# Kernel tuning notes

Hardware: AMD Instinct MI355X
Metric: run time of the kernel (lower is better)

The kernel has to match this reference:

```python
import jax, jax.numpy as jnp
import numpy as np
import math

H = 512
NH = 8
HD = H // NH


def _lin_params(key, out_dim, in_dim):
    k1, k2 = jax.random.split(key)
    bound = 1.0 / math.sqrt(in_dim)
    w = jax.random.uniform(k1, (out_dim, in_dim), minval=-bound, maxval=bound, dtype=jnp.float32)
    b = jax.random.uniform(k2, (out_dim,), minval=-bound, maxval=bound, dtype=jnp.float32)
    return w, b


def setup_inputs() -> dict:
    key = jax.random.key(0)
    ks = jax.random.split(key, 16)
    B, L = 8, 1024
    inp = {
        'hidden_states': jax.random.normal(ks[0], (B, L, H), dtype=jnp.float32),
        'text': jax.random.normal(ks[1], (B, L, H), dtype=jnp.float32),
    }
    names = ['q_img', 'k_img', 'v_img', 'q_txt', 'k_txt', 'v_txt', 'out_img', 'out_txt']
    for i, n in enumerate(names):
        w, b = _lin_params(ks[2 + i], H, H)
        inp['w_' + n] = w
        inp['b_' + n] = b
    wcat, bcat = _lin_params(ks[10], H, 2 * H)
    inp['w_cat'] = wcat
    inp['b_cat'] = bcat
    # nn.MultiheadAttention params: in_proj [3H, H], out_proj [H, H]
    inp['in_proj_w'] = jax.random.normal(ks[11], (3 * H, H), dtype=jnp.float32) * (1.0 / math.sqrt(H))
    inp['in_proj_b'] = jnp.zeros((3 * H,), dtype=jnp.float32)
    pw, pb = _lin_params(ks[12], H, H)
    inp['out_proj_w'] = pw
    inp['out_proj_b'] = pb
    return inp


def _lin(x, w, b):
    return x @ w.T + b


def _heads(x):
    B, L, _ = x.shape
    return x.reshape(B, L, NH, HD).transpose(0, 2, 1, 3)  # [B, NH, L, HD]


def _attn(q, k, v):
    # q,k,v: [B, NH, L, HD]; dropout is identity in eval mode
    scores = jnp.einsum('bhqd,bhkd->bhqk', q, k) / math.sqrt(HD)
    probs = jax.nn.softmax(scores, axis=-1)
    ctx = jnp.einsum('bhqk,bhkd->bhqd', probs, v)
    B, _, L, _ = ctx.shape
    return ctx.transpose(0, 2, 1, 3).reshape(B, L, H)


def reference(hidden_states, text,
              w_q_img, b_q_img, w_k_img, b_k_img, w_v_img, b_v_img,
              w_q_txt, b_q_txt, w_k_txt, b_k_txt, w_v_txt, b_v_txt,
              w_out_img, b_out_img, w_out_txt, b_out_txt,
              w_cat, b_cat, in_proj_w, in_proj_b, out_proj_w, out_proj_b):
    q_img = _heads(_lin(hidden_states, w_q_img, b_q_img))
    k_img = _heads(_lin(hidden_states, w_k_img, b_k_img))
    v_img = _heads(_lin(hidden_states, w_v_img, b_v_img))
    q_txt = _heads(_lin(text, w_q_txt, b_q_txt))
    k_txt = _heads(_lin(text, w_k_txt, b_k_txt))
    v_txt = _heads(_lin(text, w_v_txt, b_v_txt))

    ctx_img = _attn(q_img, k_img, v_img)
    ctx_txt = _attn(q_txt, k_txt, v_txt)
    ctx_it = _attn(q_img, k_txt, v_txt)
    ctx_ti = _attn(q_txt, k_img, v_img)

    out_img = _lin((ctx_img + ctx_it) * 0.5, w_out_img, b_out_img)
    out_txt = _lin((ctx_txt + ctx_ti) * 0.5, w_out_txt, b_out_txt)
    out = _lin(jnp.concatenate([out_img, out_txt], axis=2), w_cat, b_cat)

    # attention pooling (nn.MultiheadAttention self-attention, batch-major math)
    qkv = _lin(out, in_proj_w, in_proj_b)
    q, k, v = jnp.split(qkv, 3, axis=-1)
    ctx = _attn(_heads(q), _heads(k), _heads(v))
    return _lin(ctx, out_proj_w, out_proj_b)
```

## Files before the change

kernel.cpp:

```cpp
#include <hip/hip_runtime.h>

typedef unsigned short u16;
typedef __attribute__((ext_vector_type(4))) unsigned short u16x4;
typedef __attribute__((ext_vector_type(8))) unsigned short u16x8;
typedef __attribute__((ext_vector_type(4))) float f32x4;
typedef __attribute__((ext_vector_type(8))) __bf16 bf16x8;
typedef __attribute__((ext_vector_type(2))) unsigned int u32x2;
typedef __attribute__((ext_vector_type(4))) unsigned int u32x4;

#define WS_XH    0UL
#define WS_XT    8388608UL
#define WS_W     16777216UL
#define WS_BQI   24117248UL
#define WS_BQT   24123392UL
#define WS_QKVI  24129536UL
#define WS_QKVT  49295360UL
#define WS_VTI   74461184UL
#define WS_VTT   82849792UL
#define WS_CTXIA 91238400UL
#define WS_CTXTA 99627008UL
#define WS_OCAT  108015616UL
#define WS_OUT2  24129536UL
#define WS_QKVP  32518144UL
#define WS_VTP   57683968UL
#define WS_CTXP  66072576UL

#define SCALE_LOG2E_O8 0.18033688011112042f

__device__ __forceinline__ u16 f2bf(float f) {
  unsigned u = __float_as_uint(f);
  u += 0x7fffu + ((u >> 16) & 1u);
  return (u16)(u >> 16);
}
__device__ __forceinline__ float bf2f(u16 v) {
  return __uint_as_float(((unsigned)v) << 16);
}
__device__ __forceinline__ bf16x8 as_bf(u16x8 v) { return __builtin_bit_cast(bf16x8, v); }
__device__ __forceinline__ f32x4 mfma16(bf16x8 a, bf16x8 b, f32x4 c) {
  return __builtin_amdgcn_mfma_f32_16x16x32_bf16(a, b, c, 0, 0, 0);
}
__device__ __forceinline__ unsigned cvt_pk_bf16(float lo, float hi) {
  unsigned r;
  asm("v_cvt_pk_bf16_f32 %0, %1, %2" : "=v"(r) : "v"(lo), "v"(hi));
  return r;
}
__device__ __forceinline__ u16x8 cvt8(float4 a, float4 b) {
  u32x4 pk;
  pk[0] = cvt_pk_bf16(a.x, a.y);
  pk[1] = cvt_pk_bf16(a.z, a.w);
  pk[2] = cvt_pk_bf16(b.x, b.y);
  pk[3] = cvt_pk_bf16(b.z, b.w);
  return __builtin_bit_cast(u16x8, pk);
}

__global__ __launch_bounds__(256) void prep_weights(
    const float* __restrict__ wqi, const float* __restrict__ wki, const float* __restrict__ wvi,
    const float* __restrict__ wqt, const float* __restrict__ wkt, const float* __restrict__ wvt,
    const float* __restrict__ woi, const float* __restrict__ wot,
    const float* __restrict__ wc,  const float* __restrict__ wip, const float* __restrict__ wop,
    const float* __restrict__ bqi, const float* __restrict__ bki, const float* __restrict__ bvi,
    const float* __restrict__ bqt, const float* __restrict__ bkt, const float* __restrict__ bvt,
    u16* __restrict__ wdst, float* __restrict__ bi, float* __restrict__ bt) {
  int i = blockIdx.x * 256 + threadIdx.x;
  if (i < 786432) {
    const float* s = i < 262144 ? wqi : (i < 524288 ? wki : wvi);
    wdst[i] = f2bf(s[i & 262143]);
  } else if (i < 1572864) {
    int j = i - 786432;
    const float* s = j < 262144 ? wqt : (j < 524288 ? wkt : wvt);
    wdst[i] = f2bf(s[j & 262143]);
  } else if (i < 1835008) wdst[i] = f2bf(woi[i - 1572864]);
  else if (i < 2097152)   wdst[i] = f2bf(wot[i - 1835008]);
  else if (i < 2621440)   wdst[i] = f2bf(wc [i - 2097152]);
  else if (i < 3407872)   wdst[i] = f2bf(wip[i - 2621440]);
  else if (i < 3670016)   wdst[i] = f2bf(wop[i - 3407872]);
  else if (i < 3671552) {
    int j = i - 3670016;
    bi[j] = j < 512 ? bqi[j] : (j < 1024 ? bki[j - 512] : bvi[j - 1024]);
  } else if (i < 3673088) {
    int j = i - 3671552;
    bt[j] = j < 512 ? bqt[j] : (j < 1024 ? bkt[j - 512] : bvt[j - 1024]);
  }
}

__global__ __launch_bounds__(256) void gemm_bf16(
    const u16* __restrict__ A, const u16* __restrict__ A2, int lda, int af32,
    const u16* __restrict__ W,
    const float* __restrict__ bias, u16* __restrict__ C, int ldc, int coff, int K,
    int f32out, int qcols, float qscale, u16* __restrict__ vtout,
    long zdA, long zdA2, long zdW, long zdB, long zdC, long zdVT, int zdCoff) {
  if (blockIdx.z) {
    A += zdA;
    if (A2) A2 += zdA2;
    W += zdW; bias += zdB; C += zdC;
    if (vtout) vtout += zdVT;
    coff += zdCoff;
  }
  __shared__ __align__(16) u16 As[2][8 * 512];
  __shared__ __align__(16) u16 Bs[2][8 * 512];
  const int tid = threadIdx.x, lane = tid & 63, wv = tid >> 6;
  const int wm = wv >> 1, wn = wv & 1;
  const int ln15 = lane & 15;
  const int m0 = blockIdx.x * 128, n0 = blockIdx.y * 128;

  const int srow = lane & 15, skc = lane >> 4;
  const u16* gW0 = W + (long)(n0 + wv * 32 + srow) * K + skc * 8;
  const u16* gW1 = gW0 + (long)16 * K;

  f32x4 acc[4][4];
#pragma unroll
  for (int j = 0; j < 4; ++j) {
    float bv = bias[n0 + wn * 64 + j * 16 + ln15];
#pragma unroll
    for (int i = 0; i < 4; ++i) acc[i][j] = f32x4{bv, bv, bv, bv};
  }

  if (af32) {
    const float* fA0 = (const float*)A + (long)(m0 + wv * 32 + srow) * lda + skc * 8;
    const float* fA1 = fA0 + (long)16 * lda;
    float4 ra0a = *(const float4*)(fA0), ra0b = *(const float4*)(fA0 + 4);
    float4 ra1a = *(const float4*)(fA1), ra1b = *(const float4*)(fA1 + 4);
    u16x8 rb0 = *(const u16x8*)(gW0);
    u16x8 rb1 = *(const u16x8*)(gW1);
    int buf = 0;
    for (int k0 = 0; k0 < K; k0 += 32, buf ^= 1) {
      u16* la = As[buf] + (wv * 2) * 512;
      u16* lb = Bs[buf] + (wv * 2) * 512;
      *(u16x8*)(la + lane * 8) = cvt8(ra0a, ra0b);
      *(u16x8*)(la + 512 + lane * 8) = cvt8(ra1a, ra1b);
      *(u16x8*)(lb + lane * 8) = rb0;
      *(u16x8*)(lb + 512 + lane * 8) = rb1;
      __syncthreads();
      if (k0 + 32 < K) {
        ra0a = *(const float4*)(fA0 + k0 + 32); ra0b = *(const float4*)(fA0 + k0 + 36);
        ra1a = *(const float4*)(fA1 + k0 + 32); ra1b = *(const float4*)(fA1 + k0 + 36);
        rb0 = *(const u16x8*)(gW0 + k0 + 32);
        rb1 = *(const u16x8*)(gW1 + k0 + 32);
      }
      bf16x8 af[4], bfr[4];
#pragma unroll
      for (int i = 0; i < 4; ++i)
        af[i] = as_bf(*(const u16x8*)(As[buf] + (wm * 4 + i) * 512 + lane * 8));
#pragma unroll
      for (int j = 0; j < 4; ++j)
        bfr[j] = as_bf(*(const u16x8*)(Bs[buf] + (wn * 4 + j) * 512 + lane * 8));
#pragma unroll
      for (int i = 0; i < 4; ++i)
#pragma unroll
        for (int j = 0; j < 4; ++j) acc[i][j] = mfma16(af[i], bfr[j], acc[i][j]);
    }
  } else {
    const u16* gA0 = A + (long)(m0 + wv * 32 + srow) * lda + skc * 8;
    const u16* gA1 = gA0 + (long)16 * lda;
    const u16* gA20 = A2 + (long)(m0 + wv * 32 + srow) * lda + skc * 8;
    const u16* gA21 = gA20 + (long)16 * lda;
    u16x8 ra0 = *(const u16x8*)(gA0);
    u16x8 ra1 = *(const u16x8*)(gA1);
    u16x8 rb0 = *(const u16x8*)(gW0);
    u16x8 rb1 = *(const u16x8*)(gW1);
    u16x8 rc0, rc1;
    if (A2) { rc0 = *(const u16x8*)(gA20); rc1 = *(const u16x8*)(gA21); }
    int buf = 0;
    for (int k0 = 0; k0 < K; k0 += 32, buf ^= 1) {
      u16x8 wa0 = ra0, wa1 = ra1;
      if (A2) {
#pragma unroll
        for (int u = 0; u < 8; ++u) {
          wa0[u] = f2bf(bf2f(ra0[u]) + bf2f(rc0[u]));
          wa1[u] = f2bf(bf2f(ra1[u]) + bf2f(rc1[u]));
        }
      }
      u16* la = As[buf] + (wv * 2) * 512;
      u16* lb = Bs[buf] + (wv * 2) * 512;
      *(u16x8*)(la + lane * 8) = wa0;
      *(u16x8*)(la + 512 + lane * 8) = wa1;
      *(u16x8*)(lb + lane * 8) = rb0;
      *(u16x8*)(lb + 512 + lane * 8) = rb1;
      __syncthreads();
      if (k0 + 32 < K) {
        ra0 = *(const u16x8*)(gA0 + k0 + 32);
        ra1 = *(const u16x8*)(gA1 + k0 + 32);
        rb0 = *(const u16x8*)(gW0 + k0 + 32);
        rb1 = *(const u16x8*)(gW1 + k0 + 32);
        if (A2) { rc0 = *(const u16x8*)(gA20 + k0 + 32); rc1 = *(const u16x8*)(gA21 + k0 + 32); }
      }
      bf16x8 af[4], bfr[4];
#pragma unroll
      for (int i = 0; i < 4; ++i)
        af[i] = as_bf(*(const u16x8*)(As[buf] + (wm * 4 + i) * 512 + lane * 8));
#pragma unroll
      for (int j = 0; j < 4; ++j)
        bfr[j] = as_bf(*(const u16x8*)(Bs[buf] + (wn * 4 + j) * 512 + lane * 8));
#pragma unroll
      for (int i = 0; i < 4; ++i)
#pragma unroll
        for (int j = 0; j < 4; ++j) acc[i][j] = mfma16(af[i], bfr[j], acc[i][j]);
    }
  }
  const int quad = lane >> 4;
  const int qr4 = quad * 4;
  if (vtout && n0 >= 1024) {
#pragma unroll
    for (int j = 0; j < 4; ++j) {
      int col = n0 + wn * 64 + j * 16 + ln15;
      int dg = col - 1024;
#pragma unroll
      for (int i = 0; i < 4; ++i) {
        int row0 = m0 + wm * 64 + i * 16 + qr4;
        long vr = ((long)(row0 >> 10) * 8 + (dg >> 6)) * 64 + (dg & 63);
        u16x4 ov;
#pragma unroll
        for (int r = 0; r < 4; ++r) ov[r] = f2bf(acc[i][j][r]);
        *(u16x4*)(vtout + vr * 1024 + (row0 & 1023)) = ov;
      }
    }
    return;
  }
  float colsc[4];
#pragma unroll
  for (int j = 0; j < 4; ++j)
    colsc[j] = (n0 + wn * 64 + j * 16 < qcols) ? qscale : 1.0f;
#pragma unroll
  for (int i = 0; i < 4; ++i)
#pragma unroll
    for (int r = 0; r < 4; ++r) {
      int row = m0 + wm * 64 + i * 16 + qr4 + r;
      long cidx = (long)row * ldc + coff + n0 + wn * 64 + ln15;
      if (f32out) {
        float* cf = (float*)C + cidx;
#pragma unroll
        for (int j = 0; j < 4; ++j) cf[j * 16] = acc[i][j][r] * colsc[j];
      } else {
        u16* cp = C + cidx;
#pragma unroll
        for (int j = 0; j < 4; ++j) cp[j * 16] = f2bf(acc[i][j][r] * colsc[j]);
      }
    }
}

template <int NQF, bool DUAL>
__global__ __launch_bounds__(256) void attn_flash(
    const u16* __restrict__ Q0, const u16* __restrict__ Q1, int ldq,
    const u16* __restrict__ K0, const u16* __restrict__ VT0,
    const u16* __restrict__ K1, const u16* __restrict__ VT1, int ldk,
    u16* __restrict__ O00, u16* __restrict__ O01,
    u16* __restrict__ O10, u16* __restrict__ O11, int ldo, float outscale) {
  __shared__ __align__(16) u16 Kt[2][32][72];
  __shared__ __align__(16) u16 Vt[2][64][40];
  const int tid = threadIdx.x, lane = tid & 63, wv = tid >> 6;
  const int ln15 = lane & 15, quad = lane >> 4, q8 = quad * 8;
  const int h = blockIdx.y;

  const u16 *Q, *K, *VT;
  u16* O;
  int qtile, b;
  if constexpr (DUAL) {
    qtile = blockIdx.x >> 1;
    const int phase = blockIdx.x & 1;
    const int qsel = blockIdx.z & 1;
    b = blockIdx.z >> 1;
    Q = qsel ? Q1 : Q0;
    const int ksel = qsel ^ phase;
    K = ksel ? K1 : K0;
    VT = ksel ? VT1 : VT0;
    O = qsel ? (phase ? O11 : O10) : (phase ? O01 : O00);
  } else {
    qtile = blockIdx.x;
    b = blockIdx.z;
    Q = Q0; K = K0; VT = VT0; O = O00;
  }
  const long qrow = (long)b * 1024 + qtile * (NQF * 64) + wv * (NQF * 16);

  bf16x8 qf[NQF][2];
#pragma unroll
  for (int qi = 0; qi < NQF; ++qi) {
    const u16* qp = Q + (qrow + qi * 16 + ln15) * ldq + h * 64;
    qf[qi][0] = as_bf(*(const u16x8*)(qp + q8));
    qf[qi][1] = as_bf(*(const u16x8*)(qp + 32 + q8));
  }

  u16x8 ones_u;
#pragma unroll
  for (int j = 0; j < 8; ++j) ones_u[j] = 0x3F80;
  const bf16x8 onesb = as_bf(ones_u);

  const int kk = tid >> 3, dc = (tid & 7) * 8;
  const int vd = tid >> 2;
  const int ko = (tid & 3) * 8;
  const int vs0 = ((tid & 1) << 4) | ((tid & 2) << 1);
  const u16* Kbase = K + ((long)b * 1024 + kk) * ldk + h * 64 + dc;
  const u16* Vbase = VT + ((long)((b * 8 + h) * 64 + vd)) * 1024 + ko;

  f32x4 o[NQF][4];
  f32x4 lacc[NQF];
#pragma unroll
  for (int qi = 0; qi < NQF; ++qi) {
    lacc[qi] = f32x4{0.f, 0.f, 0.f, 0.f};
#pragma unroll
    for (int j = 0; j < 4; ++j) o[qi][j] = f32x4{0.f, 0.f, 0.f, 0.f};
  }

  u32x4 kreg = *(const u32x4*)(Kbase);
  u32x4 vreg = *(const u32x4*)(Vbase);

  int cur = 0;
  for (int k0 = 0; k0 < 1024; k0 += 32, cur ^= 1) {
    *(u32x4*)(&Kt[cur][kk][dc]) = kreg;
    u32x2 vlo = {vreg[0], vreg[1]}, vhi = {vreg[2], vreg[3]};
    *(u32x2*)(&Vt[cur][vd][vs0]) = vlo;
    *(u32x2*)(&Vt[cur][vd][vs0 + 8]) = vhi;
    __syncthreads();
    if (k0 + 32 < 1024) {
      kreg = *(const u32x4*)(Kbase + (long)(k0 + 32) * ldk);
      vreg = *(const u32x4*)(Vbase + (k0 + 32));
    }

    f32x4 st[2][NQF];
#pragma unroll
    for (int kt = 0; kt < 2; ++kt) {
      bf16x8 ka0 = as_bf(*(const u16x8*)(&Kt[cur][kt * 16 + ln15][q8]));
      bf16x8 ka1 = as_bf(*(const u16x8*)(&Kt[cur][kt * 16 + ln15][32 + q8]));
#pragma unroll
      for (int qi = 0; qi < NQF; ++qi) {
        f32x4 z = f32x4{0.f, 0.f, 0.f, 0.f};
        z = mfma16(ka0, qf[qi][0], z);
        z = mfma16(ka1, qf[qi][1], z);
        st[kt][qi] = z;
      }
    }

    bf16x8 pb[NQF];
#pragma unroll
    for (int qi = 0; qi < NQF; ++qi) {
      float p00 = __builtin_amdgcn_exp2f(st[0][qi][0]);
      float p01 = __builtin_amdgcn_exp2f(st[0][qi][1]);
      float p02 = __builtin_amdgcn_exp2f(st[0][qi][2]);
      float p03 = __builtin_amdgcn_exp2f(st[0][qi][3]);
      float p10 = __builtin_amdgcn_exp2f(st[1][qi][0]);
      float p11 = __builtin_amdgcn_exp2f(st[1][qi][1]);
      float p12 = __builtin_amdgcn_exp2f(st[1][qi][2]);
      float p13 = __builtin_amdgcn_exp2f(st[1][qi][3]);
      u32x4 pk;
      pk[0] = cvt_pk_bf16(p00, p01);
      pk[1] = cvt_pk_bf16(p02, p03);
      pk[2] = cvt_pk_bf16(p10, p11);
      pk[3] = cvt_pk_bf16(p12, p13);
      pb[qi] = as_bf(__builtin_bit_cast(u16x8, pk));
      lacc[qi] = mfma16(onesb, pb[qi], lacc[qi]);
    }
#pragma unroll
    for (int j = 0; j < 4; ++j) {
      bf16x8 av = as_bf(*(const u16x8*)(&Vt[cur][j * 16 + ln15][q8]));
#pragma unroll
      for (int qi = 0; qi < NQF; ++qi) o[qi][j] = mfma16(av, pb[qi], o[qi][j]);
    }
  }

#pragma unroll
  for (int qi = 0; qi < NQF; ++qi) {
    float inv = outscale / lacc[qi][0];
    long row = qrow + qi * 16 + ln15;
#pragma unroll
    for (int j = 0; j < 4; ++j) {
      u16x4 ov;
#pragma unroll
      for (int r = 0; r < 4; ++r) ov[r] = f2bf(o[qi][j][r] * inv);
      *(u16x4*)(O + row * ldo + h * 64 + j * 16 + quad * 4) = ov;
    }
  }
}

extern "C" void kernel_launch(void* const* d_in, const int* in_sizes, int n_in,
                              void* d_out, int out_size, void* d_ws, size_t ws_size,
                              hipStream_t stream) {
  const float* hidden = (const float*)d_in[0];
  const float* text   = (const float*)d_in[1];
  const float* wqi = (const float*)d_in[2];  const float* bqi = (const float*)d_in[3];
  const float* wki = (const float*)d_in[4];  const float* bki = (const float*)d_in[5];
  const float* wvi = (const float*)d_in[6];  const float* bvi = (const float*)d_in[7];
  const float* wqt = (const float*)d_in[8];  const float* bqt = (const float*)d_in[9];
  const float* wkt = (const float*)d_in[10]; const float* bkt = (const float*)d_in[11];
  const float* wvt = (const float*)d_in[12]; const float* bvt = (const float*)d_in[13];
  const float* woi = (const float*)d_in[14]; const float* boi = (const float*)d_in[15];
  const float* wot = (const float*)d_in[16]; const float* bot = (const float*)d_in[17];
  const float* wc  = (const float*)d_in[18]; const float* bc  = (const float*)d_in[19];
  const float* wip = (const float*)d_in[20]; const float* bip = (const float*)d_in[21];
  const float* wop = (const float*)d_in[22]; const float* bop = (const float*)d_in[23];

  char* ws = (char*)d_ws;
  u16* WB    = (u16*)(ws + WS_W);
  float* BQI = (float*)(ws + WS_BQI);
  float* BQT = (float*)(ws + WS_BQT);
  u16* QKVI  = (u16*)(ws + WS_QKVI);
  u16* QKVT  = (u16*)(ws + WS_QKVT);
  u16* VTI   = (u16*)(ws + WS_VTI);
  u16* VTT   = (u16*)(ws + WS_VTT);
  u16* CTXIA = (u16*)(ws + WS_CTXIA);
  u16* CTXIB = (u16*)(ws + WS_XH);
  u16* CTXTA = (u16*)(ws + WS_CTXTA);
  u16* CTXTB = (u16*)(ws + WS_XT);
  u16* OCAT  = (u16*)(ws + WS_OCAT);
  u16* OUT2  = (u16*)(ws + WS_OUT2);
  u16* QKVP  = (u16*)(ws + WS_QKVP);
  u16* VTP   = (u16*)(ws + WS_VTP);
  u16* CTXP  = (u16*)(ws + WS_CTXP);

  u16* WQKVI = WB;
  u16* WOUTI = WB + 1572864;
  u16* WCAT  = WB + 2097152;
  u16* WINP  = WB + 2621440;
  u16* WOUTP = WB + 3407872;

  long zdA_ht = ((const char*)text - (const char*)hidden) / 2;

  prep_weights<<<dim3(14348), 256, 0, stream>>>(wqi, wki, wvi, wqt, wkt, wvt, woi, wot,
                                                wc, wip, wop, bqi, bki, bvi, bqt, bkt, bvt,
                                                WB, BQI, BQT);
  gemm_bf16<<<dim3(64, 12, 2), 256, 0, stream>>>(
      (const u16*)hidden, nullptr, 512, 1, WQKVI, BQI, QKVI, 1536, 0, 512,
      0, 512, SCALE_LOG2E_O8, VTI,
      zdA_ht, 0, 786432, 1536, 12582912, 4194304, 0);
  attn_flash<2, true><<<dim3(16, 8, 16), 256, 0, stream>>>(
      QKVI, QKVT, 1536, QKVI + 512, VTI, QKVT + 512, VTT, 1536,
      CTXIA, CTXIB, CTXTA, CTXTB, 512, 0.5f);
  gemm_bf16<<<dim3(64, 4, 2), 256, 0, stream>>>(
      CTXIA, CTXIB, 512, 0, WOUTI, boi, OCAT, 1024, 0, 512, 0, 0, 1.0f, nullptr,
      4194304, 4194304, 262144, (long)(bot - boi),
      0, 0, 512);
  gemm_bf16<<<dim3(64, 4, 1), 256, 0, stream>>>(
      OCAT, nullptr, 1024, 0, WCAT, bc, OUT2, 512, 0, 1024, 0, 0, 1.0f, nullptr,
      0, 0, 0, 0, 0, 0, 0);
  gemm_bf16<<<dim3(64, 12, 1), 256, 0, stream>>>(
      OUT2, nullptr, 512, 0, WINP, bip, QKVP, 1536, 0, 512, 0, 512, SCALE_LOG2E_O8, VTP,
      0, 0, 0, 0, 0, 0, 0);
  attn_flash<2, false><<<dim3(8, 8, 8), 256, 0, stream>>>(
      QKVP, nullptr, 1536, QKVP + 512, VTP, nullptr, nullptr, 1536,
      CTXP, nullptr, nullptr, nullptr, 512, 1.0f);
  gemm_bf16<<<dim3(64, 4, 1), 256, 0, stream>>>(
      CTXP, nullptr, 512, 0, WOUTP, bop, (u16*)d_out, 512, 0, 512, 1, 0, 1.0f, nullptr,
      0, 0, 0, 0, 0, 0, 0);
}
```

Measured before the change: 399.3 us.

## Deepen GEMM register prefetch to two stages and barrier without vmcnt wait

The projection GEMM main loop is unrolled by two k-steps, with two register sets of global loads in flight, so prefetch runs two tiles ahead instead of one. __syncthreads is replaced by a custom barrier that waits only on LDS counters (lgkmcnt), so outstanding global loads do not stall the barrier. This aims to hide global memory latency in the linear layers. The cost is more live registers. The single barrier per step could also allow a race when a wave overwrites an LDS buffer that slower waves are still reading.

```diff
diff --git a/kernel.cpp b/kernel.cpp
--- a/kernel.cpp
+++ b/kernel.cpp
@@ -51,6 +51,9 @@
   pk[2] = cvt_pk_bf16(b.x, b.y);
   pk[3] = cvt_pk_bf16(b.z, b.w);
   return __builtin_bit_cast(u16x8, pk);
+}
+__device__ __forceinline__ void bar_novm() {
+  asm volatile("s_waitcnt lgkmcnt(0)\n\ts_barrier" ::: "memory");
 }
 
 __global__ __launch_bounds__(256) void prep_weights(
@@ -115,86 +118,124 @@
     for (int i = 0; i < 4; ++i) acc[i][j] = f32x4{bv, bv, bv, bv};
   }
 
+  auto compute = [&](int b) __attribute__((always_inline)) {
+    bf16x8 af[4], bfr[4];
+#pragma unroll
+    for (int i = 0; i < 4; ++i)
+      af[i] = as_bf(*(const u16x8*)(As[b] + (wm * 4 + i) * 512 + lane * 8));
+#pragma unroll
+    for (int j = 0; j < 4; ++j)
+      bfr[j] = as_bf(*(const u16x8*)(Bs[b] + (wn * 4 + j) * 512 + lane * 8));
+#pragma unroll
+    for (int i = 0; i < 4; ++i)
+#pragma unroll
+      for (int j = 0; j < 4; ++j) acc[i][j] = mfma16(af[i], bfr[j], acc[i][j]);
+  };
+
   if (af32) {
     const float* fA0 = (const float*)A + (long)(m0 + wv * 32 + srow) * lda + skc * 8;
     const float* fA1 = fA0 + (long)16 * lda;
-    float4 ra0a = *(const float4*)(fA0), ra0b = *(const float4*)(fA0 + 4);
-    float4 ra1a = *(const float4*)(fA1), ra1b = *(const float4*)(fA1 + 4);
-    u16x8 rb0 = *(const u16x8*)(gW0);
-    u16x8 rb1 = *(const u16x8*)(gW1);
-    int buf = 0;
-    for (int k0 = 0; k0 < K; k0 += 32, buf ^= 1) {
-      u16* la = As[buf] + (wv * 2) * 512;
-      u16* lb = Bs[buf] + (wv * 2) * 512;
-      *(u16x8*)(la + lane * 8) = cvt8(ra0a, ra0b);
-      *(u16x8*)(la + 512 + lane * 8) = cvt8(ra1a, ra1b);
-      *(u16x8*)(lb + lane * 8) = rb0;
-      *(u16x8*)(lb + 512 + lane * 8) = rb1;
-      __syncthreads();
-      if (k0 + 32 < K) {
-        ra0a = *(const float4*)(fA0 + k0 + 32); ra0b = *(const float4*)(fA0 + k0 + 36);
-        ra1a = *(const float4*)(fA1 + k0 + 32); ra1b = *(const float4*)(fA1 + k0 + 36);
-        rb0 = *(const u16x8*)(gW0 + k0 + 32);
-        rb1 = *(const u16x8*)(gW1 + k0 + 32);
-      }
-      bf16x8 af[4], bfr[4];
-#pragma unroll
-      for (int i = 0; i < 4; ++i)
-        af[i] = as_bf(*(const u16x8*)(As[buf] + (wm * 4 + i) * 512 + lane * 8));
-#pragma unroll
-      for (int j = 0; j < 4; ++j)
-        bfr[j] = as_bf(*(const u16x8*)(Bs[buf] + (wn * 4 + j) * 512 + lane * 8));
-#pragma unroll
-      for (int i = 0; i < 4; ++i)
-#pragma unroll
-        for (int j = 0; j < 4; ++j) acc[i][j] = mfma16(af[i], bfr[j], acc[i][j]);
+    float4 a00, a01, a02, a03, a10, a11, a12, a13;
+    u16x8 b00, b01, b10, b11;
+    a00 = *(const float4*)(fA0);      a01 = *(const float4*)(fA0 + 4);
+    a02 = *(const float4*)(fA1);      a03 = *(const float4*)(fA1 + 4);
+    b00 = *(const u16x8*)(gW0);       b01 = *(const u16x8*)(gW1);
+    a10 = *(const float4*)(fA0 + 32); a11 = *(const float4*)(fA0 + 36);
+    a12 = *(const float4*)(fA1 + 32); a13 = *(const float4*)(fA1 + 36);
+    b10 = *(const u16x8*)(gW0 + 32);  b11 = *(const u16x8*)(gW1 + 32);
+    for (int k0 = 0; k0 < K; k0 += 64) {
+      {
+        u16* la = As[0] + wv * 1024;
+        u16* lb = Bs[0] + wv * 1024;
+        *(u16x8*)(la + lane * 8) = cvt8(a00, a01);
+        *(u16x8*)(la + 512 + lane * 8) = cvt8(a02, a03);
+        *(u16x8*)(lb + lane * 8) = b00;
+        *(u16x8*)(lb + 512 + lane * 8) = b01;
+        bar_novm();
+        if (k0 + 64 < K) {
+          a00 = *(const float4*)(fA0 + k0 + 64); a01 = *(const float4*)(fA0 + k0 + 68);
+          a02 = *(const float4*)(fA1 + k0 + 64); a03 = *(const float4*)(fA1 + k0 + 68);
+          b00 = *(const u16x8*)(gW0 + k0 + 64);  b01 = *(const u16x8*)(gW1 + k0 + 64);
+        }
+        compute(0);
+      }
+      {
+        u16* la = As[1] + wv * 1024;
+        u16* lb = Bs[1] + wv * 1024;
+        *(u16x8*)(la + lane * 8) = cvt8(a10, a11);
+        *(u16x8*)(la + 512 + lane * 8) = cvt8(a12, a13);
+        *(u16x8*)(lb + lane * 8) = b10;
+        *(u16x8*)(lb + 512 + lane * 8) = b11;
+        bar_novm();
+        if (k0 + 96 < K) {
+          a10 = *(const float4*)(fA0 + k0 + 96); a11 = *(const float4*)(fA0 + k0 + 100);
+          a12 = *(const float4*)(fA1 + k0 + 96); a13 = *(const float4*)(fA1 + k0 + 100);
+          b10 = *(const u16x8*)(gW0 + k0 + 96);  b11 = *(const u16x8*)(gW1 + k0 + 96);
+        }
+        compute(1);
+      }
     }
   } else {
     const u16* gA0 = A + (long)(m0 + wv * 32 + srow) * lda + skc * 8;
     const u16* gA1 = gA0 + (long)16 * lda;
     const u16* gA20 = A2 + (long)(m0 + wv * 32 + srow) * lda + skc * 8;
     const u16* gA21 = gA20 + (long)16 * lda;
-    u16x8 ra0 = *(const u16x8*)(gA0);
-    u16x8 ra1 = *(const u16x8*)(gA1);
-    u16x8 rb0 = *(const u16x8*)(gW0);
-    u16x8 rb1 = *(const u16x8*)(gW1);
-    u16x8 rc0, rc1;
-    if (A2) { rc0 = *(const u16x8*)(gA20); rc1 = *(const u16x8*)(gA21); }
-    int buf = 0;
-    for (int k0 = 0; k0 < K; k0 += 32, buf ^= 1) {
-      u16x8 wa0 = ra0, wa1 = ra1;
-      if (A2) {
-#pragma unroll
-        for (int u = 0; u < 8; ++u) {
-          wa0[u] = f2bf(bf2f(ra0[u]) + bf2f(rc0[u]));
-          wa1[u] = f2bf(bf2f(ra1[u]) + bf2f(rc1[u]));
-        }
-      }
-      u16* la = As[buf] + (wv * 2) * 512;
-      u16* lb = Bs[buf] + (wv * 2) * 512;
-      *(u16x8*)(la + lane * 8) = wa0;
-      *(u16x8*)(la + 512 + lane * 8) = wa1;
-      *(u16x8*)(lb + lane * 8) = rb0;
-      *(u16x8*)(lb + 512 + lane * 8) = rb1;
-      __syncthreads();
-      if (k0 + 32 < K) {
-        ra0 = *(const u16x8*)(gA0 + k0 + 32);
-        ra1 = *(const u16x8*)(gA1 + k0 + 32);
-        rb0 = *(const u16x8*)(gW0 + k0 + 32);
-        rb1 = *(const u16x8*)(gW1 + k0 + 32);
-        if (A2) { rc0 = *(const u16x8*)(gA20 + k0 + 32); rc1 = *(const u16x8*)(gA21 + k0 + 32); }
-      }
-      bf16x8 af[4], bfr[4];
-#pragma unroll
-      for (int i = 0; i < 4; ++i)
-        af[i] = as_bf(*(const u16x8*)(As[buf] + (wm * 4 + i) * 512 + lane * 8));
-#pragma unroll
-      for (int j = 0; j < 4; ++j)
-        bfr[j] = as_bf(*(const u16x8*)(Bs[buf] + (wn * 4 + j) * 512 + lane * 8));
-#pragma unroll
-      for (int i = 0; i < 4; ++i)
-#pragma unroll
-        for (int j = 0; j < 4; ++j) acc[i][j] = mfma16(af[i], bfr[j], acc[i][j]);
+    u16x8 a00, a01, a10, a11, b00, b01, b10, b11, c00, c01, c10, c11;
+    a00 = *(const u16x8*)(gA0);      a01 = *(const u16x8*)(gA1);
+    b00 = *(const u16x8*)(gW0);      b01 = *(const u16x8*)(gW1);
+    a10 = *(const u16x8*)(gA0 + 32); a11 = *(const u16x8*)(gA1 + 32);
+    b10 = *(const u16x8*)(gW0 + 32); b11 = *(const u16x8*)(gW1 + 32);
+    if (A2) {
+      c00 = *(const u16x8*)(gA20);      c01 = *(const u16x8*)(gA21);
+      c10 = *(const u16x8*)(gA20 + 32); c11 = *(const u16x8*)(gA21 + 32);
+    }
+    for (int k0 = 0; k0 < K; k0 += 64) {
+      {
+        u16x8 wa0 = a00, wa1 = a01;
+        if (A2) {
+#pragma unroll
+          for (int u = 0; u < 8; ++u) {
+            wa0[u] = f2bf(bf2f(a00[u]) + bf2f(c00[u]));
+            wa1[u] = f2bf(bf2f(a01[u]) + bf2f(c01[u]));
+          }
+        }
+        u16* la = As[0] + wv * 1024;
+        u16* lb = Bs[0] + wv * 1024;
+        *(u16x8*)(la + lane * 8) = wa0;
+        *(u16x8*)(la + 512 + lane * 8) = wa1;
+        *(u16x8*)(lb + lane * 8) = b00;
+        *(u16x8*)(lb + 512 + lane * 8) = b01;
+        bar_novm();
+        if (k0 + 64 < K) {
+          a00 = *(const u16x8*)(gA0 + k0 + 64); a01 = *(const u16x8*)(gA1 + k0 + 64);
+          b00 = *(const u16x8*)(gW0 + k0 + 64); b01 = *(const u16x8*)(gW1 + k0 + 64);
+          if (A2) { c00 = *(const u16x8*)(gA20 + k0 + 64); c01 = *(const u16x8*)(gA21 + k0 + 64); }
+        }
+        compute(0);
+      }
+      {
+        u16x8 wa0 = a10, wa1 = a11;
+        if (A2) {
+#pragma unroll
+          for (int u = 0; u < 8; ++u) {
+            wa0[u] = f2bf(bf2f(a10[u]) + bf2f(c10[u]));
+            wa1[u] = f2bf(bf2f(a11[u]) + bf2f(c11[u]));
+          }
+        }
+        u16* la = As[1] + wv * 1024;
+        u16* lb = Bs[1] + wv * 1024;
+        *(u16x8*)(la + lane * 8) = wa0;
+        *(u16x8*)(la + 512 + lane * 8) = wa1;
+        *(u16x8*)(lb + lane * 8) = b10;
+        *(u16x8*)(lb + 512 + lane * 8) = b11;
+        bar_novm();
+        if (k0 + 96 < K) {
+          a10 = *(const u16x8*)(gA0 + k0 + 96); a11 = *(const u16x8*)(gA1 + k0 + 96);
+          b10 = *(const u16x8*)(gW0 + k0 + 96); b11 = *(const u16x8*)(gW1 + k0 + 96);
+          if (A2) { c10 = *(const u16x8*)(gA20 + k0 + 96); c11 = *(const u16x8*)(gA21 + k0 + 96); }
+        }
+        compute(1);
+      }
     }
   }
   const int quad = lane >> 4;
```

Measured after the change: 407.0 us. No clear change (+1.9%).
